# Kernel tuning notes

Hardware: AMD Instinct MI355X
Metric: run time of the kernel (lower is better)

## Reference

```python
import jax, jax.numpy as jnp
import numpy as np

B, N, H, NH = 2, 48, 256, 8
DH = H // NH  # attention head size = 32


def setup_inputs() -> dict:
    key = jax.random.key(0)
    ks = jax.random.split(key, 12)
    s = 0.02
    return {
        "attention_mask": jnp.zeros((B, 1, N, N), jnp.float32),
        "structure_matrix_pair": jax.random.normal(ks[0], (B, N, N, H), jnp.float32),
        "structure_matrix_triplet": jax.random.normal(ks[1], (B, N, N, N, H), jnp.float32),
        # Linear weights stored [in, out] (x @ W + b == torch Linear with W.T)
        "Wq": jax.random.normal(ks[2], (H, H), jnp.float32) * s, "bq": jnp.zeros((H,), jnp.float32),
        "Wk": jax.random.normal(ks[3], (H, H), jnp.float32) * s, "bk": jnp.zeros((H,), jnp.float32),
        "Wv": jax.random.normal(ks[4], (H, H), jnp.float32) * s, "bv": jnp.zeros((H,), jnp.float32),
        "Wsq": jax.random.normal(ks[5], (H, DH), jnp.float32) * s, "bsq": jnp.zeros((DH,), jnp.float32),
        "Wsk": jax.random.normal(ks[6], (H, DH), jnp.float32) * s, "bsk": jnp.zeros((DH,), jnp.float32),
        "Wsv": jax.random.normal(ks[7], (H, DH), jnp.float32) * s, "bsv": jnp.zeros((DH,), jnp.float32),
    }


def reference(attention_mask, structure_matrix_pair, structure_matrix_triplet,
              Wq, bq, Wk, bk, Wv, bv, Wsq, bsq, Wsk, bsk, Wsv, bsv):
    def heads(x):  # [B,N,N,H] -> [B,NH,N,N,DH]
        return x.reshape(B, N, N, NH, DH).transpose(0, 3, 1, 2, 4)

    q = heads(structure_matrix_pair @ Wq + bq)[:, :, :, None, :, :]  # [B,h,N,1,N,dh]
    k = heads(structure_matrix_pair @ Wk + bk)[:, :, :, :, None, :]  # [B,h,N,N,1,dh]
    v = heads(structure_matrix_pair @ Wv + bv)[:, :, :, None, :, :]  # [B,h,N,1,N,dh]

    sq = (structure_matrix_triplet @ Wsq + bsq)[:, None]  # [B,1,N,N,N,dh]
    sk = (structure_matrix_triplet @ Wsk + bsk)[:, None]
    sv = (structure_matrix_triplet @ Wsv + bsv)[:, None]

    q = q + sq  # [B,h,N,N,N,dh]
    k = k + sk
    v = v + sv

    scores = jnp.sum(q * k, axis=-1) / np.sqrt(DH).astype(np.float32)  # [B,h,N,N,N]
    scores = scores + attention_mask[:, :, None, :, :]
    probs = jax.nn.softmax(scores, axis=-1)
    # dropout is identity in eval mode
    ctx = jnp.einsum('bhikj,bhikjd->bhikd', probs, v)  # sum over last N (j)
    # [B,h,N,N,dh] -> [B,N,N,h*dh]
    return ctx.transpose(0, 2, 3, 1, 4).reshape(B, N, N, NH * DH)
```

## Files before the change

### kernel.cpp

```cpp
#include <hip/hip_runtime.h>
#include <hip/hip_bf16.h>

#define B_ 2
#define N_ 48
#define H_ 256
#define NH_ 8
#define DH_ 32
#define SQS_LD 68
#define SVT_LD 52

typedef __attribute__((ext_vector_type(8))) short bf16x8;
typedef __attribute__((ext_vector_type(4))) float f32x4;

__device__ __forceinline__ unsigned short f2bf(float f) {
  unsigned u = __float_as_uint(f);
  u += 0x7FFFu + ((u >> 16) & 1u);
  return (unsigned short)(u >> 16);
}

__device__ __forceinline__ bf16x8 cvt8(float4 x, float4 y) {
  union { unsigned u[4]; bf16x8 v; } o;
  asm("v_cvt_pk_bf16_f32 %0, %1, %2" : "=v"(o.u[0]) : "v"(x.x), "v"(x.y));
  asm("v_cvt_pk_bf16_f32 %0, %1, %2" : "=v"(o.u[1]) : "v"(x.z), "v"(x.w));
  asm("v_cvt_pk_bf16_f32 %0, %1, %2" : "=v"(o.u[2]) : "v"(y.x), "v"(y.y));
  asm("v_cvt_pk_bf16_f32 %0, %1, %2" : "=v"(o.u[3]) : "v"(y.z), "v"(y.w));
  return o.v;
}

__device__ __forceinline__ void bar_lgkm() {
  asm volatile("s_waitcnt lgkmcnt(0)" ::: "memory");
  __builtin_amdgcn_s_barrier();
  asm volatile("" ::: "memory");
}

__device__ __forceinline__ void stage48x256(const float* __restrict__ src, char* tAc, int tid) {
#pragma unroll
  for (int it = 0; it < 4; ++it) {
    int c = it * 384 + tid;
    const float4* g = reinterpret_cast<const float4*>(src) + (c << 1);
    float4 x = g[0];
    float4 y = g[1];
    int row = c >> 5;
    int off = (row << 9) + ((c & 31) << 4);
    off ^= (row & 7) << 4;
    *reinterpret_cast<bf16x8*>(tAc + off) = cvt8(x, y);
  }
}

__global__ __launch_bounds__(384, 3)
void pair_proj_kernel(const float* __restrict__ pair,
                      const float* __restrict__ Wq, const float* __restrict__ Wk,
                      const float* __restrict__ Wv, const float* __restrict__ bq,
                      const float* __restrict__ bk, const float* __restrict__ bv,
                      const float* __restrict__ Wsq, const float* __restrict__ Wsk,
                      const float* __restrict__ Wsv, const float* __restrict__ bsq,
                      const float* __restrict__ bsk, const float* __restrict__ bsv,
                      unsigned short* __restrict__ qplane, float* __restrict__ kplane,
                      unsigned short* __restrict__ vplane,
                      unsigned short* __restrict__ wfrag_main, float* __restrict__ biasm) {
  __shared__ __align__(16) char tAc[48 * 256 * 2];
  int tid = threadIdx.x;
  int lane = tid & 63;
  int wave = tid >> 6;
  int gm = blockIdx.x >> 3;
  int gn = blockIdx.x & 7;

  stage48x256(pair + (size_t)gm * 12288, tAc, tid);

  int col = gn * 96 + wave * 16 + (lane & 15);
  const float* Wsel = (col < 256) ? Wq : (col < 512) ? Wk : Wv;
  const float* bsel = (col < 256) ? bq : (col < 512) ? bk : bv;
  int cc = col & 255;
  bf16x8 wf[8];
#pragma unroll
  for (int kt = 0; kt < 8; ++kt) {
    int kbase = kt * 32 + ((lane >> 4) << 3);
    float4 w0, w1;
    w0.x = Wsel[(kbase + 0) * 256 + cc];
    w0.y = Wsel[(kbase + 1) * 256 + cc];
    w0.z = Wsel[(kbase + 2) * 256 + cc];
    w0.w = Wsel[(kbase + 3) * 256 + cc];
    w1.x = Wsel[(kbase + 4) * 256 + cc];
    w1.y = Wsel[(kbase + 5) * 256 + cc];
    w1.z = Wsel[(kbase + 6) * 256 + cc];
    w1.w = Wsel[(kbase + 7) * 256 + cc];
    wf[kt] = cvt8(w0, w1);
  }
  float bias = bsel[cc];

  if (gn == 7) {
    if (tid < 256) {
      int p = gm * 256 + tid;
      int i8 = p & 7, l2 = (p >> 3) & 63, kt2 = (p >> 9) & 7, nt2 = p >> 12;
      int k2 = kt2 * 32 + ((l2 >> 4) << 3) + i8;
      int n2 = nt2 * 16 + (l2 & 15);
      const float* W = (n2 < 32) ? Wsq : (n2 < 64) ? Wsk : Wsv;
      wfrag_main[p] = f2bf(W[k2 * 32 + (n2 & 31)]);
    } else if (gm == 0 && tid < 352) {
      int p = tid - 256;
      biasm[p] = (p < 32) ? bsq[p] : (p < 64) ? bsk[p - 32] : bsv[p - 64];
    }
  }
  __syncthreads();

  f32x4 acc[3];
#pragma unroll
  for (int mt = 0; mt < 3; ++mt) acc[mt] = (f32x4){0.f, 0.f, 0.f, 0.f};
#pragma unroll
  for (int kt = 0; kt < 8; ++kt) {
#pragma unroll
    for (int mt = 0; mt < 3; ++mt) {
      int row = mt * 16 + (lane & 15);
      int off = (row << 9) + (kt << 6) + ((lane >> 4) << 4);
      off ^= (row & 7) << 4;
      bf16x8 a = *reinterpret_cast<const bf16x8*>(tAc + off);
      acc[mt] = __builtin_amdgcn_mfma_f32_16x16x32_bf16(a, wf[kt], acc[mt], 0, 0, 0);
    }
  }

  int jb = (lane >> 4) * 4;
#pragma unroll
  for (int mt = 0; mt < 3; ++mt) {
#pragma unroll
    for (int rr = 0; rr < 4; ++rr) {
      int j = mt * 16 + jb + rr;
      size_t row = (size_t)(gm * 48 + j) * 256;
      float val = acc[mt][rr] + bias;
      if (col < 256) qplane[row + col] = f2bf(val);
      else if (col < 512) kplane[row + (col - 256)] = val;
      else vplane[row + (col - 512)] = f2bf(val);
    }
  }
}

__global__ __launch_bounds__(384, 6)
void e2e_fused(const float* __restrict__ mask, const float* __restrict__ trip,
               const unsigned short* __restrict__ qplane, const float* __restrict__ kplane,
               const unsigned short* __restrict__ vplane,
               const unsigned short* __restrict__ wfragm,
               const float* __restrict__ biasm, float* __restrict__ out) {
  __shared__ __align__(16) char smem[48 * 256 * 2];
  __shared__ __align__(16) float svT[32 * SVT_LD];
  __shared__ __align__(16) float khl[256];
  __shared__ __align__(16) float pbuf[8][48];
  char* tAc = smem;
  float* sqS = reinterpret_cast<float*>(smem);

  int tid = threadIdx.x;
  int lane = tid & 63;
  int wave = tid >> 6;

  int bid = blockIdx.x;
  int s = (bid & 7) * 576 + (bid >> 3);
  int g = s / 48;
  int k = s % 48;
  int b = g / 48;
  int rowbase = g * 48;

  if (tid < 256) khl[tid] = kplane[(size_t)s * 256 + tid];

  const float4* src = reinterpret_cast<const float4*>(trip + (size_t)s * 12288);
  int r0 = tid >> 4, c0 = tid & 15;
  int r1 = (384 + tid) >> 4, c1 = tid & 15;
  float4 pa[4], pb[4];
  pa[0] = src[r0 * 64 + c0 * 2];
  pa[1] = src[r0 * 64 + c0 * 2 + 1];
  pa[2] = src[r1 * 64 + c1 * 2];
  pa[3] = src[r1 * 64 + c1 * 2 + 1];
  pb[0] = src[r0 * 64 + 32 + c0 * 2];
  pb[1] = src[r0 * 64 + 32 + c0 * 2 + 1];
  pb[2] = src[r1 * 64 + 32 + c1 * 2];
  pb[3] = src[r1 * 64 + 32 + c1 * 2 + 1];

  {
    int off0 = (r0 << 9) + (c0 << 4);
    off0 ^= (r0 & 7) << 4;
    *reinterpret_cast<bf16x8*>(tAc + off0) = cvt8(pa[0], pa[1]);
    int off1 = (r1 << 9) + (c1 << 4);
    off1 ^= (r1 & 7) << 4;
    *reinterpret_cast<bf16x8*>(tAc + off1) = cvt8(pa[2], pa[3]);
  }
  bar_lgkm();

  const bf16x8* wp = reinterpret_cast<const bf16x8*>(wfragm);
  f32x4 acc[3];
#pragma unroll
  for (int mt = 0; mt < 3; ++mt) acc[mt] = (f32x4){0.f, 0.f, 0.f, 0.f};
#pragma unroll
  for (int kt = 0; kt < 4; ++kt) {
    bf16x8 w = wp[(wave * 8 + kt) * 64 + lane];
#pragma unroll
    for (int mt = 0; mt < 3; ++mt) {
      int row = mt * 16 + (lane & 15);
      int off = (row << 9) + (kt << 6) + ((lane >> 4) << 4);
      off ^= (row & 7) << 4;
      bf16x8 a = *reinterpret_cast<const bf16x8*>(tAc + off);
      acc[mt] = __builtin_amdgcn_mfma_f32_16x16x32_bf16(a, w, acc[mt], 0, 0, 0);
    }
  }
  {
    int off0 = (r0 << 9) + ((16 + c0) << 4);
    off0 ^= (r0 & 7) << 4;
    *reinterpret_cast<bf16x8*>(tAc + off0) = cvt8(pb[0], pb[1]);
    int off1 = (r1 << 9) + ((16 + c1) << 4);
    off1 ^= (r1 & 7) << 4;
    *reinterpret_cast<bf16x8*>(tAc + off1) = cvt8(pb[2], pb[3]);
  }
  bar_lgkm();

#pragma unroll
  for (int kt = 4; kt < 8; ++kt) {
    bf16x8 w = wp[(wave * 8 + kt) * 64 + lane];
#pragma unroll
    for (int mt = 0; mt < 3; ++mt) {
      int row = mt * 16 + (lane & 15);
      int off = (row << 9) + (kt << 6) + ((lane >> 4) << 4);
      off ^= (row & 7) << 4;
      bf16x8 a = *reinterpret_cast<const bf16x8*>(tAc + off);
      acc[mt] = __builtin_amdgcn_mfma_f32_16x16x32_bf16(a, w, acc[mt], 0, 0, 0);
    }
  }
  bar_lgkm();

  {
    int n = wave * 16 + (lane & 15);
    float bias = biasm[n];
    int jb = (lane >> 4) * 4;
    if (wave < 4) {
#pragma unroll
      for (int mt = 0; mt < 3; ++mt) {
#pragma unroll
        for (int rr = 0; rr < 4; ++rr)
          sqS[(mt * 16 + jb + rr) * SQS_LD + n] = acc[mt][rr] + bias;
      }
    } else {
      int d = n - 64;
#pragma unroll
      for (int mt = 0; mt < 3; ++mt) {
#pragma unroll
        for (int rr = 0; rr < 4; ++rr)
          svT[d * SVT_LD + mt * 16 + jb + rr] = acc[mt][rr] + bias;
      }
    }
  }
  bar_lgkm();

  {
    int j = tid >> 3, dq = tid & 7;
    float4 sq = *reinterpret_cast<const float4*>(sqS + j * SQS_LD + dq * 4);
    float4 sk = *reinterpret_cast<const float4*>(sqS + j * SQS_LD + 32 + dq * 4);
    const unsigned short* qrow = qplane + (size_t)(rowbase + j) * 256;
    float val[8];
#pragma unroll
    for (int h = 0; h < 8; ++h) {
      uint2 qw = *reinterpret_cast<const uint2*>(qrow + h * 32 + dq * 4);
      float4 kh = *reinterpret_cast<const float4*>(khl + h * 32 + dq * 4);
      float v = (__uint_as_float(qw.x << 16) + sq.x) * (kh.x + sk.x);
      v += (__uint_as_float(qw.x & 0xFFFF0000u) + sq.y) * (kh.y + sk.y);
      v += (__uint_as_float(qw.y << 16) + sq.z) * (kh.z + sk.z);
      v += (__uint_as_float(qw.y & 0xFFFF0000u) + sq.w) * (kh.w + sk.w);
      val[h] = v;
    }
#pragma unroll
    for (int h = 0; h < 8; ++h) {
      val[h] += __shfl_xor(val[h], 1);
      val[h] += __shfl_xor(val[h], 2);
      val[h] += __shfl_xor(val[h], 4);
    }
    float sc = val[0];
#pragma unroll
    for (int h = 1; h < 8; ++h) sc = (dq == h) ? val[h] : sc;
    pbuf[dq][j] = sc * 0.17677669529663687f + mask[b * 2304 + k * 48 + j];
  }
  bar_lgkm();

  for (int h = wave; h < 8; h += 6) {
    float x = (lane < 48) ? pbuf[h][lane] : -INFINITY;
    float m = x;
#pragma unroll
    for (int off = 32; off; off >>= 1) m = fmaxf(m, __shfl_xor(m, off));
    float e = (lane < 48) ? __expf(x - m) : 0.f;
    float sum = e;
#pragma unroll
    for (int off = 32; off; off >>= 1) sum += __shfl_xor(sum, off);
    if (lane < 48) pbuf[h][lane] = e / sum;
  }
  bar_lgkm();

  if (tid < 256) {
    int h = tid >> 5, d = tid & 31;
    const unsigned short* vbase = vplane + (size_t)rowbase * 256 + tid;
    float a = 0.f;
#pragma unroll
    for (int j4 = 0; j4 < 12; ++j4) {
      float4 p4 = *reinterpret_cast<const float4*>(&pbuf[h][j4 * 4]);
      float4 sv4 = *reinterpret_cast<const float4*>(svT + d * SVT_LD + j4 * 4);
      float v0 = __uint_as_float((unsigned)vbase[(size_t)(j4 * 4 + 0) * 256] << 16);
      float v1 = __uint_as_float((unsigned)vbase[(size_t)(j4 * 4 + 1) * 256] << 16);
      float v2 = __uint_as_float((unsigned)vbase[(size_t)(j4 * 4 + 2) * 256] << 16);
      float v3 = __uint_as_float((unsigned)vbase[(size_t)(j4 * 4 + 3) * 256] << 16);
      a += p4.x * (v0 + sv4.x);
      a += p4.y * (v1 + sv4.y);
      a += p4.z * (v2 + sv4.z);
      a += p4.w * (v3 + sv4.w);
    }
    out[(size_t)s * 256 + tid] = a;
  }
}

extern "C" void kernel_launch(void* const* d_in, const int* in_sizes, int n_in,
                              void* d_out, int out_size, void* d_ws, size_t ws_size,
                              hipStream_t stream) {
  const float* mask = (const float*)d_in[0];
  const float* pair = (const float*)d_in[1];
  const float* trip = (const float*)d_in[2];
  const float* Wq = (const float*)d_in[3];
  const float* bq = (const float*)d_in[4];
  const float* Wk = (const float*)d_in[5];
  const float* bk = (const float*)d_in[6];
  const float* Wv = (const float*)d_in[7];
  const float* bv = (const float*)d_in[8];
  const float* Wsq = (const float*)d_in[9];
  const float* bsq = (const float*)d_in[10];
  const float* Wsk = (const float*)d_in[11];
  const float* bsk = (const float*)d_in[12];
  const float* Wsv = (const float*)d_in[13];
  const float* bsv = (const float*)d_in[14];

  char* ws = (char*)d_ws;
  unsigned short* qplane = (unsigned short*)ws;
  float* kplane = (float*)(ws + 2359296);
  unsigned short* vplane = (unsigned short*)(ws + 7077888);
  unsigned short* wfrag_main = (unsigned short*)(ws + 9437184);
  float* biasm = (float*)(ws + 9486336);

  pair_proj_kernel<<<768, 384, 0, stream>>>(pair, Wq, Wk, Wv, bq, bk, bv,
                                            Wsq, Wsk, Wsv, bsq, bsk, bsv,
                                            qplane, kplane, vplane,
                                            wfrag_main, biasm);
  e2e_fused<<<4608, 384, 0, stream>>>(mask, trip, qplane, kplane, vplane,
                                      wfrag_main, biasm, (float*)d_out);
}
```

Baseline: 72.30 us.

## Interleave Q/K/V projections into one bf16 buffer and fuse softmax with PV

The pair projection now writes Q, K and V interleaved into a single bf16 buffer with a row stride of 768, and K is stored in bf16 instead of fp32. The attention kernel reads from this combined buffer and prefetches the mask value early. Softmax and the probability-times-V stage now run in the same four waves, with only a local LDS wait between them instead of a block barrier. This cuts workspace traffic and removes one barrier, at the cost of some K precision and strided V reads that are less coalesced.

```diff
diff --git a/kernel.cpp b/kernel.cpp
--- a/kernel.cpp
+++ b/kernel.cpp
@@ -55,8 +55,7 @@
                       const float* __restrict__ Wsq, const float* __restrict__ Wsk,
                       const float* __restrict__ Wsv, const float* __restrict__ bsq,
                       const float* __restrict__ bsk, const float* __restrict__ bsv,
-                      unsigned short* __restrict__ qplane, float* __restrict__ kplane,
-                      unsigned short* __restrict__ vplane,
+                      unsigned short* __restrict__ pqkv,
                       unsigned short* __restrict__ wfrag_main, float* __restrict__ biasm) {
   __shared__ __align__(16) char tAc[48 * 256 * 2];
   int tid = threadIdx.x;
@@ -124,19 +123,14 @@
 #pragma unroll
     for (int rr = 0; rr < 4; ++rr) {
       int j = mt * 16 + jb + rr;
-      size_t row = (size_t)(gm * 48 + j) * 256;
-      float val = acc[mt][rr] + bias;
-      if (col < 256) qplane[row + col] = f2bf(val);
-      else if (col < 512) kplane[row + (col - 256)] = val;
-      else vplane[row + (col - 512)] = f2bf(val);
+      pqkv[(size_t)(gm * 48 + j) * 768 + col] = f2bf(acc[mt][rr] + bias);
     }
   }
 }
 
 __global__ __launch_bounds__(384, 6)
 void e2e_fused(const float* __restrict__ mask, const float* __restrict__ trip,
-               const unsigned short* __restrict__ qplane, const float* __restrict__ kplane,
-               const unsigned short* __restrict__ vplane,
+               const unsigned short* __restrict__ pqkv,
                const unsigned short* __restrict__ wfragm,
                const float* __restrict__ biasm, float* __restrict__ out) {
   __shared__ __align__(16) char smem[48 * 256 * 2];
@@ -157,7 +151,12 @@
   int b = g / 48;
   int rowbase = g * 48;
 
-  if (tid < 256) khl[tid] = kplane[(size_t)s * 256 + tid];
+  float maskr = mask[b * 2304 + k * 48 + (tid >> 3)];
+
+  if (tid < 256) {
+    unsigned short kv = pqkv[(size_t)s * 768 + 256 + tid];
+    khl[tid] = __uint_as_float((unsigned)kv << 16);
+  }
 
   const float4* src = reinterpret_cast<const float4*>(trip + (size_t)s * 12288);
   int r0 = tid >> 4, c0 = tid & 15;
@@ -249,7 +248,7 @@
     int j = tid >> 3, dq = tid & 7;
     float4 sq = *reinterpret_cast<const float4*>(sqS + j * SQS_LD + dq * 4);
     float4 sk = *reinterpret_cast<const float4*>(sqS + j * SQS_LD + 32 + dq * 4);
-    const unsigned short* qrow = qplane + (size_t)(rowbase + j) * 256;
+    const unsigned short* qrow = pqkv + (size_t)(rowbase + j) * 768;
     float val[8];
 #pragma unroll
     for (int h = 0; h < 8; ++h) {
@@ -270,35 +269,37 @@
     float sc = val[0];
 #pragma unroll
     for (int h = 1; h < 8; ++h) sc = (dq == h) ? val[h] : sc;
-    pbuf[dq][j] = sc * 0.17677669529663687f + mask[b * 2304 + k * 48 + j];
-  }
-  bar_lgkm();
-
-  for (int h = wave; h < 8; h += 6) {
-    float x = (lane < 48) ? pbuf[h][lane] : -INFINITY;
-    float m = x;
-#pragma unroll
-    for (int off = 32; off; off >>= 1) m = fmaxf(m, __shfl_xor(m, off));
-    float e = (lane < 48) ? __expf(x - m) : 0.f;
-    float sum = e;
-#pragma unroll
-    for (int off = 32; off; off >>= 1) sum += __shfl_xor(sum, off);
-    if (lane < 48) pbuf[h][lane] = e / sum;
-  }
-  bar_lgkm();
-
-  if (tid < 256) {
+    pbuf[dq][j] = sc * 0.17677669529663687f + maskr;
+  }
+  bar_lgkm();
+
+  if (wave < 4) {
+#pragma unroll
+    for (int hh = 0; hh < 2; ++hh) {
+      int h = wave * 2 + hh;
+      float x = (lane < 48) ? pbuf[h][lane] : -INFINITY;
+      float m = x;
+#pragma unroll
+      for (int off = 32; off; off >>= 1) m = fmaxf(m, __shfl_xor(m, off));
+      float e = (lane < 48) ? __expf(x - m) : 0.f;
+      float sum = e;
+#pragma unroll
+      for (int off = 32; off; off >>= 1) sum += __shfl_xor(sum, off);
+      if (lane < 48) pbuf[h][lane] = e / sum;
+    }
+    asm volatile("s_waitcnt lgkmcnt(0)" ::: "memory");
+
     int h = tid >> 5, d = tid & 31;
-    const unsigned short* vbase = vplane + (size_t)rowbase * 256 + tid;
+    const unsigned short* vbase = pqkv + (size_t)rowbase * 768 + 512 + tid % 256;
     float a = 0.f;
 #pragma unroll
     for (int j4 = 0; j4 < 12; ++j4) {
       float4 p4 = *reinterpret_cast<const float4*>(&pbuf[h][j4 * 4]);
       float4 sv4 = *reinterpret_cast<const float4*>(svT + d * SVT_LD + j4 * 4);
-      float v0 = __uint_as_float((unsigned)vbase[(size_t)(j4 * 4 + 0) * 256] << 16);
-      float v1 = __uint_as_float((unsigned)vbase[(size_t)(j4 * 4 + 1) * 256] << 16);
-      float v2 = __uint_as_float((unsigned)vbase[(size_t)(j4 * 4 + 2) * 256] << 16);
-      float v3 = __uint_as_float((unsigned)vbase[(size_t)(j4 * 4 + 3) * 256] << 16);
+      float v0 = __uint_as_float((unsigned)vbase[(size_t)(j4 * 4 + 0) * 768] << 16);
+      float v1 = __uint_as_float((unsigned)vbase[(size_t)(j4 * 4 + 1) * 768] << 16);
+      float v2 = __uint_as_float((unsigned)vbase[(size_t)(j4 * 4 + 2) * 768] << 16);
+      float v3 = __uint_as_float((unsigned)vbase[(size_t)(j4 * 4 + 3) * 768] << 16);
       a += p4.x * (v0 + sv4.x);
       a += p4.y * (v1 + sv4.y);
       a += p4.z * (v2 + sv4.z);
@@ -328,16 +329,13 @@
   const float* bsv = (const float*)d_in[14];
 
   char* ws = (char*)d_ws;
-  unsigned short* qplane = (unsigned short*)ws;
-  float* kplane = (float*)(ws + 2359296);
-  unsigned short* vplane = (unsigned short*)(ws + 7077888);
-  unsigned short* wfrag_main = (unsigned short*)(ws + 9437184);
-  float* biasm = (float*)(ws + 9486336);
+  unsigned short* pqkv = (unsigned short*)ws;
+  unsigned short* wfrag_main = (unsigned short*)(ws + 7077888);
+  float* biasm = (float*)(ws + 7127040);
 
   pair_proj_kernel<<<768, 384, 0, stream>>>(pair, Wq, Wk, Wv, bq, bk, bv,
                                             Wsq, Wsk, Wsv, bsq, bsk, bsv,
-                                            qplane, kplane, vplane,
-                                            wfrag_main, biasm);
-  e2e_fused<<<4608, 384, 0, stream>>>(mask, trip, qplane, kplane, vplane,
-                                      wfrag_main, biasm, (float*)d_out);
-}
+                                            pqkv, wfrag_main, biasm);
+  e2e_fused<<<4608, 384, 0, stream>>>(mask, trip, pqkv, wfrag_main, biasm,
+                                      (float*)d_out);
+}
```

Result: no change. 71.19 us (-1.5%).
